# Kernel tuning notes

Hardware: AMD Instinct MI355X
Metric: run time of the kernel (lower is better)

Reference implementation:

```python
import jax, jax.numpy as jnp
import numpy as np

H = 8          # num_heads
KD = 64        # key_dim
R = 256        # num_random_features
EPS = 1e-3     # kernel_epsilon
SCALE = 1.0 / np.sqrt(KD)
CHUNK = 128    # chunk size for causal scan (math identical to full cumsum)


def setup_inputs() -> dict:
    key = jax.random.key(0)
    ks = jax.random.split(key, 7)
    B, S, D = 4, 4096, H * KD
    x = jax.random.normal(ks[0], (B, S, D), dtype=jnp.float32)
    Wq = jax.random.normal(ks[1], (D, D), dtype=jnp.float32) * 0.02
    Wk = jax.random.normal(ks[2], (D, D), dtype=jnp.float32) * 0.02
    Wv = jax.random.normal(ks[3], (D, D), dtype=jnp.float32) * 0.02
    Wo = jax.random.normal(ks[4], (D, D), dtype=jnp.float32) * 0.02
    bo = jnp.zeros((D,), dtype=jnp.float32)
    # random_features: orthogonal rows within each KD block (keras 'orthogonal' init approx)
    g = jax.random.normal(ks[5], (R, KD), dtype=jnp.float32)
    rf = jnp.concatenate([jnp.linalg.qr(b.T)[0].T for b in g.reshape(R // KD, KD, KD)], axis=0)
    return {"x": x, "Wq": Wq, "Wk": Wk, "Wv": Wv, "Wo": Wo, "bo": bo, "rf": rf}


def _kernel_features(z, rf):
    # z: [B,S,H,KD] -> [B,S,H,R]; scale applied AFTER projection as in source
    p = jnp.einsum('bshd,rd->bshr', z, rf) * SCALE
    p = p - jnp.max(p, axis=-1, keepdims=True)
    return jnp.exp(p) + EPS


def _causal_favor(qf, kf, v):
    # qf,kf: [B,S,H,R]; v: [B,S,H,KD]. Equivalent to cumsum of bshrd outer products.
    B, S, _, _ = qf.shape
    nc = S // CHUNK
    def to_chunks(t):
        return jnp.moveaxis(t.reshape(B, nc, CHUNK, *t.shape[2:]), 1, 0)
    qc_all, kc_all, vc_all = to_chunks(qf), to_chunks(kf), to_chunks(v)

    @jax.checkpoint
    def step(carry, inp):
        S0, Z0 = carry                     # S0: [B,H,R,KD], Z0: [B,H,R]
        qc, kc, vc = inp                   # [B,C,H,R], [B,C,H,R], [B,C,H,KD]
        kv = jnp.einsum('bchr,bchd->bchrd', kc, vc)
        kv_cum = jnp.cumsum(kv, axis=1) + S0[:, None]
        num = jnp.einsum('bchr,bchrd->bchd', qc, kv_cum)
        z_cum = jnp.cumsum(kc, axis=1) + Z0[:, None]
        den = jnp.einsum('bchr,bchr->bch', qc, z_cum) + EPS
        out = num / den[..., None]
        return (kv_cum[:, -1], z_cum[:, -1]), out

    S0 = jnp.zeros((B, H, R, KD), dtype=qf.dtype)
    Z0 = jnp.zeros((B, H, R), dtype=qf.dtype)
    _, outs = jax.lax.scan(step, (S0, Z0), (qc_all, kc_all, vc_all))
    return jnp.moveaxis(outs, 0, 1).reshape(B, S, H, KD)


def reference(x, Wq, Wk, Wv, Wo, bo, rf):
    B, S, D = x.shape
    q = (x @ Wq).reshape(B, S, H, KD)
    k = (x @ Wk).reshape(B, S, H, KD)
    v = (x @ Wv).reshape(B, S, H, KD)
    qf = _kernel_features(q, rf)
    kf = _kernel_features(k, rf)
    attn = _causal_favor(qf, kf, v)        # [B,S,H,KD]
    attn = attn.reshape(B, S, H * KD)
    return attn @ Wo + bo
```

## Files before the change

kernel.cpp:

```cpp
#include <hip/hip_runtime.h>
#include <stdint.h>


namespace {
constexpr int kB = 4;
constexpr int kS = 4096;
constexpr int kH = 8;
constexpr int kD = 512;
constexpr int kR = 256;
constexpr int kNC = 32;
constexpr float kEPS = 1e-3f;
constexpr int kSP = 80;
constexpr int kSST = kSP * 256;
}

typedef __attribute__((ext_vector_type(8))) short bf16x8;
typedef __attribute__((ext_vector_type(4))) float f32x4;

__device__ __forceinline__ f32x4 mfma16(bf16x8 a, bf16x8 b, f32x4 c) {
  return __builtin_amdgcn_mfma_f32_16x16x32_bf16(a, b, c, 0, 0, 0);
}

__device__ __forceinline__ uint16_t f2bf(float x) {
  union { float f; uint32_t i; } c; c.f = x;
  uint32_t r = c.i + 0x7fffu + ((c.i >> 16) & 1u);
  return (uint16_t)(r >> 16);
}

__global__ __launch_bounds__(256) void cast_inputs(
    const float* __restrict__ x, const float* __restrict__ rfm,
    uint16_t* __restrict__ x16, uint16_t* __restrict__ rf16)
{
  int i4 = blockIdx.x * 256 + threadIdx.x;
  const int n1 = 2097152;
  const int n2 = 4096;
  const float* src; uint16_t* dst; int off;
  if (i4 < n1) { src = x; dst = x16; off = i4; }
  else if (i4 < n1 + n2) { src = rfm; dst = rf16; off = i4 - n1; }
  else return;
  float4 v = *(const float4*)(src + (size_t)off * 4);
  uint2 o;
  o.x = (uint32_t)f2bf(v.x) | ((uint32_t)f2bf(v.y) << 16);
  o.y = (uint32_t)f2bf(v.z) | ((uint32_t)f2bf(v.w) << 16);
  *(uint2*)(dst + (size_t)off * 4) = o;
}

__global__ __launch_bounds__(256) void transpose_w(
    const float* __restrict__ Wq, const float* __restrict__ Wk,
    const float* __restrict__ Wv, const float* __restrict__ Wo,
    uint16_t* __restrict__ WtBase)
{
  __shared__ uint16_t t16[64][72];
  const int z = blockIdx.z;
  const float* W = (z == 0) ? Wq : (z == 1) ? Wk : (z == 2) ? Wv : Wo;
  uint16_t* Wt = WtBase + (size_t)z * 262144;
  const int tid = threadIdx.x;
  const int k0 = blockIdx.x * 64, n0 = blockIdx.y * 64;
#pragma unroll
  for (int i = 0; i < 4; ++i) {
    int idx = tid + 256 * i;
    int kk = idx >> 4, nn4 = (idx & 15) * 4;
    float4 v = *(const float4*)(W + (size_t)(k0 + kk) * 512 + n0 + nn4);
    t16[kk][nn4 + 0] = f2bf(v.x);
    t16[kk][nn4 + 1] = f2bf(v.y);
    t16[kk][nn4 + 2] = f2bf(v.z);
    t16[kk][nn4 + 3] = f2bf(v.w);
  }
  __syncthreads();
#pragma unroll
  for (int i = 0; i < 4; ++i) {
    int idx = tid + 256 * i;
    int nn = idx >> 4, kk4 = (idx & 15) * 4;
    uint2 o;
    o.x = (uint32_t)t16[kk4 + 0][nn] | ((uint32_t)t16[kk4 + 1][nn] << 16);
    o.y = (uint32_t)t16[kk4 + 2][nn] | ((uint32_t)t16[kk4 + 3][nn] << 16);
    *(uint2*)(Wt + (size_t)(n0 + nn) * 512 + k0 + kk4) = o;
  }
}

template <bool BF16OUT>
__global__ __launch_bounds__(256) void gemm_bf16(
    const uint16_t* __restrict__ A, const uint16_t* __restrict__ Bt,
    const float* __restrict__ bias, void* __restrict__ O)
{
  const int tid = threadIdx.x;
  const int w = tid >> 6, lane = tid & 63;
  const int lr = lane & 15, lg = lane >> 4;
  const int m_base = blockIdx.x * 128 + w * 32;
  const int n_base = blockIdx.y * 64;

  f32x4 acc[2][4];
#pragma unroll
  for (int mf = 0; mf < 2; ++mf)
#pragma unroll
    for (int nf = 0; nf < 4; ++nf) acc[mf][nf] = (f32x4){0.f, 0.f, 0.f, 0.f};

  const uint16_t* a0p = A + (size_t)(m_base + lr) * 512 + 8 * lg;
  const uint16_t* a1p = a0p + (size_t)16 * 512;
  const uint16_t* bp = Bt + (size_t)(n_base + lr) * 512 + 8 * lg;

#pragma unroll
  for (int ks = 0; ks < 16; ++ks) {
    bf16x8 a0 = *(const bf16x8*)(a0p + ks * 32);
    bf16x8 a1 = *(const bf16x8*)(a1p + ks * 32);
#pragma unroll
    for (int nf = 0; nf < 4; ++nf) {
      bf16x8 b = *(const bf16x8*)(bp + (size_t)nf * 16 * 512 + ks * 32);
      acc[0][nf] = mfma16(a0, b, acc[0][nf]);
      acc[1][nf] = mfma16(a1, b, acc[1][nf]);
    }
  }

  float badd[4];
#pragma unroll
  for (int nf = 0; nf < 4; ++nf)
    badd[nf] = bias ? bias[n_base + nf * 16 + lr] : 0.0f;

  if constexpr (BF16OUT) {
    __shared__ uint16_t tr[4][32][72];
#pragma unroll
    for (int mf = 0; mf < 2; ++mf)
#pragma unroll
      for (int nf = 0; nf < 4; ++nf)
#pragma unroll
        for (int reg = 0; reg < 4; ++reg)
          tr[w][mf * 16 + 4 * lg + reg][nf * 16 + lr] = f2bf(acc[mf][nf][reg] + badd[nf]);
    __syncthreads();
#pragma unroll
    for (int it = 0; it < 4; ++it) {
      int idx = it * 64 + lane;
      int row = idx >> 3, c8 = (idx & 7) * 8;
      uint4 val = *(const uint4*)&tr[w][row][c8];
      *(uint4*)((uint16_t*)O + (size_t)(m_base + row) * 512 + n_base + c8) = val;
    }
  } else {
    __shared__ float trf[4][32][68];
#pragma unroll
    for (int mf = 0; mf < 2; ++mf)
#pragma unroll
      for (int nf = 0; nf < 4; ++nf)
#pragma unroll
        for (int reg = 0; reg < 4; ++reg)
          trf[w][mf * 16 + 4 * lg + reg][nf * 16 + lr] = acc[mf][nf][reg] + badd[nf];
    __syncthreads();
#pragma unroll
    for (int it = 0; it < 8; ++it) {
      int idx = it * 64 + lane;
      int row = idx >> 4, c4 = (idx & 15) * 4;
      float4 val = *(const float4*)&trf[w][row][c4];
      *(float4*)((float*)O + (size_t)(m_base + row) * 512 + n_base + c4) = val;
    }
  }
}

__global__ __launch_bounds__(256) void gemm_feat(
    const uint16_t* __restrict__ x16, const uint16_t* __restrict__ WtBase,
    const uint16_t* __restrict__ rf16,
    uint16_t* __restrict__ qf, uint16_t* __restrict__ kf)
{
  __shared__ uint16_t trbuf[4][2176];

  const uint16_t* Bt = WtBase + (size_t)blockIdx.z * 262144;
  uint16_t* dst = blockIdx.z ? kf : qf;
  const int h = blockIdx.y;
  const int tid = threadIdx.x;
  const int w = tid >> 6, lane = tid & 63;
  const int lr = lane & 15, lg = lane >> 4;
  const int m_base = blockIdx.x * 128 + w * 32;

  f32x4 acc[2][4];
#pragma unroll
  for (int mf = 0; mf < 2; ++mf)
#pragma unroll
    for (int nf = 0; nf < 4; ++nf) acc[mf][nf] = (f32x4){0.f, 0.f, 0.f, 0.f};

  const uint16_t* a0p = x16 + (size_t)(m_base + lr) * 512 + 8 * lg;
  const uint16_t* a1p = a0p + (size_t)16 * 512;
  const uint16_t* bp = Bt + (size_t)(h * 64 + lr) * 512 + 8 * lg;

#pragma unroll
  for (int ks = 0; ks < 16; ++ks) {
    bf16x8 a0 = *(const bf16x8*)(a0p + ks * 32);
    bf16x8 a1 = *(const bf16x8*)(a1p + ks * 32);
#pragma unroll
    for (int nf = 0; nf < 4; ++nf) {
      bf16x8 b = *(const bf16x8*)(bp + (size_t)nf * 16 * 512 + ks * 32);
      acc[0][nf] = mfma16(a0, b, acc[0][nf]);
      acc[1][nf] = mfma16(a1, b, acc[1][nf]);
    }
  }

  uint16_t (*trw)[72] = (uint16_t (*)[72])&trbuf[w][0];
  bf16x8 qa[2][2];
#pragma unroll
  for (int mf = 0; mf < 2; ++mf) {
#pragma unroll
    for (int nf = 0; nf < 4; ++nf)
#pragma unroll
      for (int reg = 0; reg < 4; ++reg)
        trw[4 * lg + reg][nf * 16 + lr] = f2bf(acc[mf][nf][reg] * 0.125f);
    qa[mf][0] = *(const bf16x8*)&trw[lr][8 * lg];
    qa[mf][1] = *(const bf16x8*)&trw[lr][32 + 8 * lg];
  }

  f32x4 acc2[2][16];
#pragma unroll
  for (int mf = 0; mf < 2; ++mf)
#pragma unroll
    for (int nf = 0; nf < 16; ++nf) acc2[mf][nf] = (f32x4){0.f, 0.f, 0.f, 0.f};
#pragma unroll
  for (int ks = 0; ks < 2; ++ks) {
#pragma unroll
    for (int nf = 0; nf < 16; ++nf) {
      bf16x8 b = *(const bf16x8*)(rf16 + (size_t)(nf * 16 + lr) * 64 + ks * 32 + 8 * lg);
      acc2[0][nf] = mfma16(qa[0][ks], b, acc2[0][nf]);
      acc2[1][nf] = mfma16(qa[1][ks], b, acc2[1][nf]);
    }
  }

  uint16_t (*trh)[136] = (uint16_t (*)[136])&trbuf[w][0];
#pragma unroll
  for (int mf = 0; mf < 2; ++mf) {
    float mx[4] = {-1e30f, -1e30f, -1e30f, -1e30f};
#pragma unroll
    for (int nf = 0; nf < 16; ++nf)
#pragma unroll
      for (int reg = 0; reg < 4; ++reg)
        mx[reg] = fmaxf(mx[reg], acc2[mf][nf][reg]);
#pragma unroll
    for (int reg = 0; reg < 4; ++reg) {
      mx[reg] = fmaxf(mx[reg], __shfl_xor(mx[reg], 1));
      mx[reg] = fmaxf(mx[reg], __shfl_xor(mx[reg], 2));
      mx[reg] = fmaxf(mx[reg], __shfl_xor(mx[reg], 4));
      mx[reg] = fmaxf(mx[reg], __shfl_xor(mx[reg], 8));
    }
#pragma unroll
    for (int half = 0; half < 2; ++half) {
#pragma unroll
      for (int nf8 = 0; nf8 < 8; ++nf8) {
        int nf = half * 8 + nf8;
#pragma unroll
        for (int reg = 0; reg < 4; ++reg)
          trh[4 * lg + reg][nf8 * 16 + lr] =
              f2bf(__expf(acc2[mf][nf][reg] - mx[reg]) + kEPS);
      }
#pragma unroll
      for (int it = 0; it < 4; ++it) {
        int idx = it * 64 + lane;
        int row = idx >> 4, c8 = (idx & 15) * 8;
        uint4 val = *(const uint4*)&trh[row][c8];
        size_t t = (size_t)m_base + mf * 16 + row;
        *(uint4*)(dst + (t * 8 + h) * 256 + half * 128 + c8) = val;
      }
    }
  }
}

__global__ __launch_bounds__(256) void chunk_mfma(
    const uint16_t* __restrict__ kfeat, const uint16_t* __restrict__ vbuf,
    uint16_t* __restrict__ Skv)
{
  __shared__ uint16_t Vaug[80][136];
  __shared__ uint16_t uni2[21120];
  uint16_t (*kfT)[72] = (uint16_t (*)[72])uni2;
  uint16_t (*outT)[264] = (uint16_t (*)[264])uni2;

  const int c = blockIdx.x, bh = blockIdx.y;
  const int b = bh >> 3, h = bh & 7;
  const int tid = threadIdx.x;
  const int w = tid >> 6, lane = tid & 63;
  const int lr = lane & 15, lg = lane >> 4;
  const size_t srow = (size_t)b * kS + (size_t)c * 128;

#pragma unroll
  for (int i = 0; i < 4; ++i) {
    int idx = tid + 256 * i;
    int u = idx & 127, d = (idx >> 7) * 8;
    uint4 w8 = *(const uint4*)(vbuf + (srow + u) * kD + h * 64 + d);
    Vaug[d + 0][u] = (uint16_t)(w8.x & 0xffff);
    Vaug[d + 1][u] = (uint16_t)(w8.x >> 16);
    Vaug[d + 2][u] = (uint16_t)(w8.y & 0xffff);
    Vaug[d + 3][u] = (uint16_t)(w8.y >> 16);
    Vaug[d + 4][u] = (uint16_t)(w8.z & 0xffff);
    Vaug[d + 5][u] = (uint16_t)(w8.z >> 16);
    Vaug[d + 6][u] = (uint16_t)(w8.w & 0xffff);
    Vaug[d + 7][u] = (uint16_t)(w8.w >> 16);
  }
  if (tid < 128) Vaug[64][tid] = 0x3F80;
  if (tid < 136) {
#pragma unroll
    for (int rr = 65; rr < 80; ++rr) Vaug[rr][tid] = 0;
  }

  f32x4 acc[5][4];
#pragma unroll
  for (int mf = 0; mf < 5; ++mf)
#pragma unroll
    for (int nf = 0; nf < 4; ++nf) acc[mf][nf] = (f32x4){0.f, 0.f, 0.f, 0.f};

  const uint16_t* kp0 = kfeat + (srow * kH + h) * kR;
#pragma unroll
  for (int th = 0; th < 2; ++th) {
    if (th) __syncthreads();
    const uint16_t* kp = kp0 + (size_t)th * 64 * (kH * kR);
#pragma unroll
    for (int i = 0; i < 16; ++i) {
      int idx = tid + 256 * i;
      int t = idx >> 6, c4 = idx & 63;
      uint2 wv = *(const uint2*)(kp + (size_t)t * (kH * kR) + c4 * 4);
      int r = c4 * 4;
      kfT[r + 0][t] = (uint16_t)(wv.x & 0xffff);
      kfT[r + 1][t] = (uint16_t)(wv.x >> 16);
      kfT[r + 2][t] = (uint16_t)(wv.y & 0xffff);
      kfT[r + 3][t] = (uint16_t)(wv.y >> 16);
    }
    __syncthreads();
#pragma unroll
    for (int ks = 0; ks < 2; ++ks) {
      bf16x8 af[5];
#pragma unroll
      for (int mf = 0; mf < 5; ++mf)
        af[mf] = *(const bf16x8*)&Vaug[mf * 16 + lr][th * 64 + ks * 32 + 8 * lg];
#pragma unroll
      for (int nf = 0; nf < 4; ++nf) {
        bf16x8 kb = *(const bf16x8*)&kfT[w * 64 + nf * 16 + lr][ks * 32 + 8 * lg];
#pragma unroll
        for (int mf = 0; mf < 5; ++mf)
          acc[mf][nf] = mfma16(af[mf], kb, acc[mf][nf]);
      }
    }
  }

  __syncthreads();
#pragma unroll
  for (int mf = 0; mf < 5; ++mf)
#pragma unroll
    for (int nf = 0; nf < 4; ++nf)
#pragma unroll
      for (int reg = 0; reg < 4; ++reg)
        outT[mf * 16 + 4 * lg + reg][w * 64 + nf * 16 + lr] = f2bf(acc[mf][nf][reg]);
  __syncthreads();

  uint16_t* So = Skv + ((size_t)bh * kNC + c) * kSST;
#pragma unroll
  for (int it = 0; it < 10; ++it) {
    int idx = tid + 256 * it;
    int row = idx >> 5, c8 = (idx & 31) * 8;
    uint4 val = *(const uint4*)&outT[row][c8];
    *(uint4*)(So + (size_t)row * 256 + c8) = val;
  }
}

__global__ __launch_bounds__(256) void prefix_kernel(uint16_t* __restrict__ Skv)
{
  int e = blockIdx.x * 256 + threadIdx.x;
  int bh = e / kSST;
  int rd = e - bh * kSST;
  size_t base = (size_t)bh * kNC * kSST + rd;
  float run = 0.f;
  for (int c = 0; c < kNC; ++c) {
    size_t idx = base + (size_t)c * kSST;
    union { uint32_t i; float f; } cv; cv.i = ((uint32_t)Skv[idx]) << 16;
    Skv[idx] = f2bf(run);
    run += cv.f;
  }
}

__global__ __launch_bounds__(256) void favor_mfma(
    const uint16_t* __restrict__ qfeat, const uint16_t* __restrict__ kfeat,
    const uint16_t* __restrict__ vbuf, const uint16_t* __restrict__ Skv,
    uint16_t* __restrict__ attn16)
{
  __shared__ uint16_t Vaug[80][136];
  __shared__ uint16_t A_l[4][32][40];

  const int c = blockIdx.x, bh = blockIdx.y;
  const int b = bh >> 3, h = bh & 7;
  const int tid = threadIdx.x;
  const int w = tid >> 6, lane = tid & 63;
  const int lr = lane & 15, lg = lane >> 4;
  const size_t srow = (size_t)b * kS + (size_t)c * 128;

#pragma unroll
  for (int i = 0; i < 4; ++i) {
    int idx = tid + 256 * i;
    int u = idx & 127, d = (idx >> 7) * 8;
    uint4 w8 = *(const uint4*)(vbuf + (srow + u) * kD + h * 64 + d);
    Vaug[d + 0][u] = (uint16_t)(w8.x & 0xffff);
    Vaug[d + 1][u] = (uint16_t)(w8.x >> 16);
    Vaug[d + 2][u] = (uint16_t)(w8.y & 0xffff);
    Vaug[d + 3][u] = (uint16_t)(w8.y >> 16);
    Vaug[d + 4][u] = (uint16_t)(w8.z & 0xffff);
    Vaug[d + 5][u] = (uint16_t)(w8.z >> 16);
    Vaug[d + 6][u] = (uint16_t)(w8.w & 0xffff);
    Vaug[d + 7][u] = (uint16_t)(w8.w >> 16);
  }
  if (tid < 128) Vaug[64][tid] = 0x3F80;
  if (tid < 136) {
#pragma unroll
    for (int rr = 65; rr < 80; ++rr) Vaug[rr][tid] = 0;
  }

  bf16x8 qa[2][8];
  const uint16_t* qp = qfeat + ((srow + w * 32 + lr) * kH + h) * kR + 8 * lg;
#pragma unroll
  for (int mf = 0; mf < 2; ++mf)
#pragma unroll
    for (int ks = 0; ks < 8; ++ks)
      qa[mf][ks] = *(const bf16x8*)(qp + (size_t)mf * 16 * (kH * kR) + ks * 32);

  f32x4 o[2][5];
#pragma unroll
  for (int mf = 0; mf < 2; ++mf)
#pragma unroll
    for (int nf = 0; nf < 5; ++nf) o[mf][nf] = (f32x4){0.f, 0.f, 0.f, 0.f};

  const uint16_t* Sg = Skv + ((size_t)bh * kNC + c) * kSST + 8 * lg;
#pragma unroll
  for (int ks = 0; ks < 8; ++ks) {
#pragma unroll
    for (int nf = 0; nf < 5; ++nf) {
      bf16x8 sb = *(const bf16x8*)(Sg + (size_t)(nf * 16 + lr) * 256 + ks * 32);
      o[0][nf] = mfma16(qa[0][ks], sb, o[0][nf]);
      o[1][nf] = mfma16(qa[1][ks], sb, o[1][nf]);
    }
  }

  __syncthreads();

  const uint16_t* kp = kfeat + (srow + lr) * (kH * kR) + h * kR + 8 * lg;
  for (int ut = 0; ut <= w; ++ut) {
    f32x4 aacc[2][2];
#pragma unroll
    for (int mf = 0; mf < 2; ++mf)
#pragma unroll
      for (int nf = 0; nf < 2; ++nf) aacc[mf][nf] = (f32x4){0.f, 0.f, 0.f, 0.f};
#pragma unroll
    for (int ks = 0; ks < 8; ++ks) {
      bf16x8 kb0 = *(const bf16x8*)(kp + (size_t)(ut * 32) * (kH * kR) + ks * 32);
      bf16x8 kb1 = *(const bf16x8*)(kp + (size_t)(ut * 32 + 16) * (kH * kR) + ks * 32);
      aacc[0][0] = mfma16(qa[0][ks], kb0, aacc[0][0]);
      aacc[0][1] = mfma16(qa[0][ks], kb1, aacc[0][1]);
      aacc[1][0] = mfma16(qa[1][ks], kb0, aacc[1][0]);
      aacc[1][1] = mfma16(qa[1][ks], kb1, aacc[1][1]);
    }
#pragma unroll
    for (int mf = 0; mf < 2; ++mf)
#pragma unroll
      for (int nf = 0; nf < 2; ++nf)
#pragma unroll
        for (int reg = 0; reg < 4; ++reg) {
          int trow = mf * 16 + 4 * lg + reg;
          int ucol = nf * 16 + lr;
          float v = aacc[mf][nf][reg];
          if (ut == w && ucol > trow) v = 0.0f;
          A_l[w][trow][ucol] = f2bf(v);
        }
    bf16x8 af0 = *(const bf16x8*)&A_l[w][lr][8 * lg];
    bf16x8 af1 = *(const bf16x8*)&A_l[w][16 + lr][8 * lg];
#pragma unroll
    for (int nf = 0; nf < 5; ++nf) {
      bf16x8 vb = *(const bf16x8*)&Vaug[nf * 16 + lr][ut * 32 + 8 * lg];
      o[0][nf] = mfma16(af0, vb, o[0][nf]);
      o[1][nf] = mfma16(af1, vb, o[1][nf]);
    }
  }

#pragma unroll
  for (int mf = 0; mf < 2; ++mf) {
    float inv[4];
#pragma unroll
    for (int reg = 0; reg < 4; ++reg) {
      float den = __shfl(o[mf][4][reg], lane & 48);
      inv[reg] = 1.0f / (den + kEPS);
    }
    const size_t trow = srow + w * 32 + mf * 16 + 4 * lg;
#pragma unroll
    for (int reg = 0; reg < 4; ++reg) {
      uint16_t* op = attn16 + (trow + reg) * kD + h * 64 + lr;
#pragma unroll
      for (int nf = 0; nf < 4; ++nf)
        op[nf * 16] = f2bf(o[mf][nf][reg] * inv[reg]);
    }
  }
}

extern "C" void kernel_launch(void* const* d_in, const int* in_sizes, int n_in,
                              void* d_out, int out_size, void* d_ws, size_t ws_size,
                              hipStream_t stream)
{
  (void)in_sizes; (void)n_in; (void)out_size; (void)ws_size;
  const float* x  = (const float*)d_in[0];
  const float* Wq = (const float*)d_in[1];
  const float* Wk = (const float*)d_in[2];
  const float* Wv = (const float*)d_in[3];
  const float* Wo = (const float*)d_in[4];
  const float* bo = (const float*)d_in[5];
  const float* rf = (const float*)d_in[6];
  float* out = (float*)d_out;

  const size_t MiB = 1048576;
  char* ws = (char*)d_ws;
  uint16_t* x16    = (uint16_t*)ws;
  uint16_t* attn16 = (uint16_t*)(ws + 16 * MiB);
  uint16_t* v16    = (uint16_t*)(ws + 32 * MiB);
  uint16_t* qf     = (uint16_t*)(ws + 48 * MiB);
  uint16_t* kf     = (uint16_t*)(ws + 112 * MiB);
  uint16_t* Skv    = (uint16_t*)(ws + 176 * MiB);
  uint16_t* Wt     = (uint16_t*)(ws + 216 * MiB);
  uint16_t* rf16   = (uint16_t*)(ws + 218 * MiB);

  cast_inputs<<<dim3(8208, 1, 1), 256, 0, stream>>>(x, rf, x16, rf16);
  transpose_w<<<dim3(8, 8, 4), 256, 0, stream>>>(Wq, Wk, Wv, Wo, Wt);

  gemm_feat<<<dim3(128, 8, 2), 256, 0, stream>>>(x16, Wt, rf16, qf, kf);

  gemm_bf16<true><<<dim3(128, 8, 1), 256, 0, stream>>>(x16, Wt + 2 * 262144, nullptr, v16);

  chunk_mfma<<<dim3(kNC, kB * kH, 1), 256, 0, stream>>>(kf, v16, Skv);
  prefix_kernel<<<dim3(2560, 1, 1), 256, 0, stream>>>(Skv);
  favor_mfma<<<dim3(kNC, kB * kH, 1), 256, 0, stream>>>(qf, kf, v16, Skv, attn16);

  gemm_bf16<false><<<dim3(128, 8, 1), 256, 0, stream>>>(attn16, Wt + 3 * 262144, bo, out);
}
```

Measured before the change: 381.7 us.

## Store q/k features and V head-major; halve feature GEMM tile; stage attn output stores

Moves qf, kf and v16 from a [B,S,H,*] layout to a head-major [B,H,S,*] layout, so the per-(b,h) chunk kernels read contiguous rows instead of rows strided by H. gemm_feat now gives each wave a 16-row tile, so twice as many blocks are launched and fewer accumulator registers are live per thread. favor_mfma now stages its output through shared memory and writes 16-byte coalesced stores instead of scattered 2-byte stores. The x rows in gemm_feat are reused less, and an extra barrier is added before the output stage.

```diff
diff --git a/kernel.cpp b/kernel.cpp
--- a/kernel.cpp
+++ b/kernel.cpp
@@ -126,12 +126,15 @@
         for (int reg = 0; reg < 4; ++reg)
           tr[w][mf * 16 + 4 * lg + reg][nf * 16 + lr] = f2bf(acc[mf][nf][reg] + badd[nf]);
     __syncthreads();
+    const int h = blockIdx.y;
 #pragma unroll
     for (int it = 0; it < 4; ++it) {
       int idx = it * 64 + lane;
       int row = idx >> 3, c8 = (idx & 7) * 8;
       uint4 val = *(const uint4*)&tr[w][row][c8];
-      *(uint4*)((uint16_t*)O + (size_t)(m_base + row) * 512 + n_base + c8) = val;
+      int m = m_base + row;
+      int b = m >> 12, t = m & 4095;
+      *(uint4*)((uint16_t*)O + ((size_t)(b * 8 + h) * 4096 + t) * 64 + c8) = val;
     }
   } else {
     __shared__ float trf[4][32][68];
@@ -158,7 +161,7 @@
     const uint16_t* __restrict__ rf16,
     uint16_t* __restrict__ qf, uint16_t* __restrict__ kf)
 {
-  __shared__ uint16_t trbuf[4][2176];
+  __shared__ uint16_t trbuf[4][16][72];
 
   const uint16_t* Bt = WtBase + (size_t)blockIdx.z * 262144;
   uint16_t* dst = blockIdx.z ? kf : qf;
@@ -166,92 +169,76 @@
   const int tid = threadIdx.x;
   const int w = tid >> 6, lane = tid & 63;
   const int lr = lane & 15, lg = lane >> 4;
-  const int m_base = blockIdx.x * 128 + w * 32;
-
-  f32x4 acc[2][4];
-#pragma unroll
-  for (int mf = 0; mf < 2; ++mf)
-#pragma unroll
-    for (int nf = 0; nf < 4; ++nf) acc[mf][nf] = (f32x4){0.f, 0.f, 0.f, 0.f};
+  const int m_base = blockIdx.x * 64 + w * 16;
+  const int b = m_base >> 12, tloc = m_base & 4095;
+
+  f32x4 acc[4];
+#pragma unroll
+  for (int nf = 0; nf < 4; ++nf) acc[nf] = (f32x4){0.f, 0.f, 0.f, 0.f};
 
   const uint16_t* a0p = x16 + (size_t)(m_base + lr) * 512 + 8 * lg;
-  const uint16_t* a1p = a0p + (size_t)16 * 512;
   const uint16_t* bp = Bt + (size_t)(h * 64 + lr) * 512 + 8 * lg;
 
 #pragma unroll
   for (int ks = 0; ks < 16; ++ks) {
     bf16x8 a0 = *(const bf16x8*)(a0p + ks * 32);
-    bf16x8 a1 = *(const bf16x8*)(a1p + ks * 32);
 #pragma unroll
     for (int nf = 0; nf < 4; ++nf) {
       bf16x8 b = *(const bf16x8*)(bp + (size_t)nf * 16 * 512 + ks * 32);
-      acc[0][nf] = mfma16(a0, b, acc[0][nf]);
-      acc[1][nf] = mfma16(a1, b, acc[1][nf]);
-    }
-  }
-
-  uint16_t (*trw)[72] = (uint16_t (*)[72])&trbuf[w][0];
-  bf16x8 qa[2][2];
-#pragma unroll
-  for (int mf = 0; mf < 2; ++mf) {
-#pragma unroll
-    for (int nf = 0; nf < 4; ++nf)
+      acc[nf] = mfma16(a0, b, acc[nf]);
+    }
+  }
+
+  uint16_t (*trw)[72] = trbuf[w];
+#pragma unroll
+  for (int nf = 0; nf < 4; ++nf)
+#pragma unroll
+    for (int reg = 0; reg < 4; ++reg)
+      trw[4 * lg + reg][nf * 16 + lr] = f2bf(acc[nf][reg] * 0.125f);
+  bf16x8 qa0 = *(const bf16x8*)&trw[lr][8 * lg];
+  bf16x8 qa1 = *(const bf16x8*)&trw[lr][32 + 8 * lg];
+
+  f32x4 acc2[16];
+#pragma unroll
+  for (int nf = 0; nf < 16; ++nf) acc2[nf] = (f32x4){0.f, 0.f, 0.f, 0.f};
+#pragma unroll
+  for (int nf = 0; nf < 16; ++nf) {
+    bf16x8 b0 = *(const bf16x8*)(rf16 + (size_t)(nf * 16 + lr) * 64 + 8 * lg);
+    bf16x8 b1 = *(const bf16x8*)(rf16 + (size_t)(nf * 16 + lr) * 64 + 32 + 8 * lg);
+    acc2[nf] = mfma16(qa0, b0, acc2[nf]);
+    acc2[nf] = mfma16(qa1, b1, acc2[nf]);
+  }
+
+  float mx[4] = {-1e30f, -1e30f, -1e30f, -1e30f};
+#pragma unroll
+  for (int nf = 0; nf < 16; ++nf)
+#pragma unroll
+    for (int reg = 0; reg < 4; ++reg)
+      mx[reg] = fmaxf(mx[reg], acc2[nf][reg]);
+#pragma unroll
+  for (int reg = 0; reg < 4; ++reg) {
+    mx[reg] = fmaxf(mx[reg], __shfl_xor(mx[reg], 1));
+    mx[reg] = fmaxf(mx[reg], __shfl_xor(mx[reg], 2));
+    mx[reg] = fmaxf(mx[reg], __shfl_xor(mx[reg], 4));
+    mx[reg] = fmaxf(mx[reg], __shfl_xor(mx[reg], 8));
+  }
+  uint16_t* dbase = dst + ((size_t)(b * 8 + h) * 4096 + tloc) * 256;
+#pragma unroll
+  for (int qtr = 0; qtr < 4; ++qtr) {
+#pragma unroll
+    for (int nf4 = 0; nf4 < 4; ++nf4) {
+      int nf = qtr * 4 + nf4;
 #pragma unroll
       for (int reg = 0; reg < 4; ++reg)
-        trw[4 * lg + reg][nf * 16 + lr] = f2bf(acc[mf][nf][reg] * 0.125f);
-    qa[mf][0] = *(const bf16x8*)&trw[lr][8 * lg];
-    qa[mf][1] = *(const bf16x8*)&trw[lr][32 + 8 * lg];
-  }
-
-  f32x4 acc2[2][16];
-#pragma unroll
-  for (int mf = 0; mf < 2; ++mf)
-#pragma unroll
-    for (int nf = 0; nf < 16; ++nf) acc2[mf][nf] = (f32x4){0.f, 0.f, 0.f, 0.f};
-#pragma unroll
-  for (int ks = 0; ks < 2; ++ks) {
-#pragma unroll
-    for (int nf = 0; nf < 16; ++nf) {
-      bf16x8 b = *(const bf16x8*)(rf16 + (size_t)(nf * 16 + lr) * 64 + ks * 32 + 8 * lg);
-      acc2[0][nf] = mfma16(qa[0][ks], b, acc2[0][nf]);
-      acc2[1][nf] = mfma16(qa[1][ks], b, acc2[1][nf]);
-    }
-  }
-
-  uint16_t (*trh)[136] = (uint16_t (*)[136])&trbuf[w][0];
-#pragma unroll
-  for (int mf = 0; mf < 2; ++mf) {
-    float mx[4] = {-1e30f, -1e30f, -1e30f, -1e30f};
-#pragma unroll
-    for (int nf = 0; nf < 16; ++nf)
-#pragma unroll
-      for (int reg = 0; reg < 4; ++reg)
-        mx[reg] = fmaxf(mx[reg], acc2[mf][nf][reg]);
-#pragma unroll
-    for (int reg = 0; reg < 4; ++reg) {
-      mx[reg] = fmaxf(mx[reg], __shfl_xor(mx[reg], 1));
-      mx[reg] = fmaxf(mx[reg], __shfl_xor(mx[reg], 2));
-      mx[reg] = fmaxf(mx[reg], __shfl_xor(mx[reg], 4));
-      mx[reg] = fmaxf(mx[reg], __shfl_xor(mx[reg], 8));
-    }
-#pragma unroll
-    for (int half = 0; half < 2; ++half) {
-#pragma unroll
-      for (int nf8 = 0; nf8 < 8; ++nf8) {
-        int nf = half * 8 + nf8;
-#pragma unroll
-        for (int reg = 0; reg < 4; ++reg)
-          trh[4 * lg + reg][nf8 * 16 + lr] =
-              f2bf(__expf(acc2[mf][nf][reg] - mx[reg]) + kEPS);
-      }
-#pragma unroll
-      for (int it = 0; it < 4; ++it) {
-        int idx = it * 64 + lane;
-        int row = idx >> 4, c8 = (idx & 15) * 8;
-        uint4 val = *(const uint4*)&trh[row][c8];
-        size_t t = (size_t)m_base + mf * 16 + row;
-        *(uint4*)(dst + (t * 8 + h) * 256 + half * 128 + c8) = val;
-      }
+        trw[4 * lg + reg][nf4 * 16 + lr] =
+            f2bf(__expf(acc2[nf][reg] - mx[reg]) + kEPS);
+    }
+#pragma unroll
+    for (int it = 0; it < 2; ++it) {
+      int idx = it * 64 + lane;
+      int row = idx >> 3, c8 = (idx & 7) * 8;
+      uint4 val = *(const uint4*)&trw[row][c8];
+      *(uint4*)(dbase + (size_t)row * 256 + qtr * 64 + c8) = val;
     }
   }
 }
@@ -266,17 +253,16 @@
   uint16_t (*outT)[264] = (uint16_t (*)[264])uni2;
 
   const int c = blockIdx.x, bh = blockIdx.y;
-  const int b = bh >> 3, h = bh & 7;
   const int tid = threadIdx.x;
   const int w = tid >> 6, lane = tid & 63;
   const int lr = lane & 15, lg = lane >> 4;
-  const size_t srow = (size_t)b * kS + (size_t)c * 128;
+  const size_t vrow = (size_t)bh * 4096 + (size_t)c * 128;
 
 #pragma unroll
   for (int i = 0; i < 4; ++i) {
     int idx = tid + 256 * i;
     int u = idx & 127, d = (idx >> 7) * 8;
-    uint4 w8 = *(const uint4*)(vbuf + (srow + u) * kD + h * 64 + d);
+    uint4 w8 = *(const uint4*)(vbuf + (vrow + u) * 64 + d);
     Vaug[d + 0][u] = (uint16_t)(w8.x & 0xffff);
     Vaug[d + 1][u] = (uint16_t)(w8.x >> 16);
     Vaug[d + 2][u] = (uint16_t)(w8.y & 0xffff);
@@ -298,16 +284,16 @@
 #pragma unroll
     for (int nf = 0; nf < 4; ++nf) acc[mf][nf] = (f32x4){0.f, 0.f, 0.f, 0.f};
 
-  const uint16_t* kp0 = kfeat + (srow * kH + h) * kR;
+  const uint16_t* kp0 = kfeat + vrow * 256;
 #pragma unroll
   for (int th = 0; th < 2; ++th) {
     if (th) __syncthreads();
-    const uint16_t* kp = kp0 + (size_t)th * 64 * (kH * kR);
+    const uint16_t* kp = kp0 + (size_t)th * 64 * 256;
 #pragma unroll
     for (int i = 0; i < 16; ++i) {
       int idx = tid + 256 * i;
       int t = idx >> 6, c4 = idx & 63;
-      uint2 wv = *(const uint2*)(kp + (size_t)t * (kH * kR) + c4 * 4);
+      uint2 wv = *(const uint2*)(kp + (size_t)t * 256 + c4 * 4);
       int r = c4 * 4;
       kfT[r + 0][t] = (uint16_t)(wv.x & 0xffff);
       kfT[r + 1][t] = (uint16_t)(wv.x >> 16);
@@ -379,13 +365,14 @@
   const int tid = threadIdx.x;
   const int w = tid >> 6, lane = tid & 63;
   const int lr = lane & 15, lg = lane >> 4;
+  const size_t vrow = (size_t)bh * 4096 + (size_t)c * 128;
   const size_t srow = (size_t)b * kS + (size_t)c * 128;
 
 #pragma unroll
   for (int i = 0; i < 4; ++i) {
     int idx = tid + 256 * i;
     int u = idx & 127, d = (idx >> 7) * 8;
-    uint4 w8 = *(const uint4*)(vbuf + (srow + u) * kD + h * 64 + d);
+    uint4 w8 = *(const uint4*)(vbuf + (vrow + u) * 64 + d);
     Vaug[d + 0][u] = (uint16_t)(w8.x & 0xffff);
     Vaug[d + 1][u] = (uint16_t)(w8.x >> 16);
     Vaug[d + 2][u] = (uint16_t)(w8.y & 0xffff);
@@ -402,12 +389,12 @@
   }
 
   bf16x8 qa[2][8];
-  const uint16_t* qp = qfeat + ((srow + w * 32 + lr) * kH + h) * kR + 8 * lg;
+  const uint16_t* qp = qfeat + (vrow + w * 32 + lr) * 256 + 8 * lg;
 #pragma unroll
   for (int mf = 0; mf < 2; ++mf)
 #pragma unroll
     for (int ks = 0; ks < 8; ++ks)
-      qa[mf][ks] = *(const bf16x8*)(qp + (size_t)mf * 16 * (kH * kR) + ks * 32);
+      qa[mf][ks] = *(const bf16x8*)(qp + (size_t)mf * 16 * 256 + ks * 32);
 
   f32x4 o[2][5];
 #pragma unroll
@@ -428,7 +415,7 @@
 
   __syncthreads();
 
-  const uint16_t* kp = kfeat + (srow + lr) * (kH * kR) + h * kR + 8 * lg;
+  const uint16_t* kp = kfeat + (vrow + lr) * 256 + 8 * lg;
   for (int ut = 0; ut <= w; ++ut) {
     f32x4 aacc[2][2];
 #pragma unroll
@@ -437,8 +424,8 @@
       for (int nf = 0; nf < 2; ++nf) aacc[mf][nf] = (f32x4){0.f, 0.f, 0.f, 0.f};
 #pragma unroll
     for (int ks = 0; ks < 8; ++ks) {
-      bf16x8 kb0 = *(const bf16x8*)(kp + (size_t)(ut * 32) * (kH * kR) + ks * 32);
-      bf16x8 kb1 = *(const bf16x8*)(kp + (size_t)(ut * 32 + 16) * (kH * kR) + ks * 32);
+      bf16x8 kb0 = *(const bf16x8*)(kp + (size_t)(ut * 32) * 256 + ks * 32);
+      bf16x8 kb1 = *(const bf16x8*)(kp + (size_t)(ut * 32 + 16) * 256 + ks * 32);
       aacc[0][0] = mfma16(qa[0][ks], kb0, aacc[0][0]);
       aacc[0][1] = mfma16(qa[0][ks], kb1, aacc[0][1]);
       aacc[1][0] = mfma16(qa[1][ks], kb0, aacc[1][0]);
@@ -466,6 +453,8 @@
     }
   }
 
+  __syncthreads();
+  uint16_t (*osc)[72] = (uint16_t (*)[72])&Vaug[0][0];
 #pragma unroll
   for (int mf = 0; mf < 2; ++mf) {
     float inv[4];
@@ -474,14 +463,20 @@
       float den = __shfl(o[mf][4][reg], lane & 48);
       inv[reg] = 1.0f / (den + kEPS);
     }
-    const size_t trow = srow + w * 32 + mf * 16 + 4 * lg;
-#pragma unroll
-    for (int reg = 0; reg < 4; ++reg) {
-      uint16_t* op = attn16 + (trow + reg) * kD + h * 64 + lr;
-#pragma unroll
-      for (int nf = 0; nf < 4; ++nf)
-        op[nf * 16] = f2bf(o[mf][nf][reg] * inv[reg]);
-    }
+#pragma unroll
+    for (int nf = 0; nf < 4; ++nf)
+#pragma unroll
+      for (int reg = 0; reg < 4; ++reg)
+        osc[w * 32 + mf * 16 + 4 * lg + reg][nf * 16 + lr] =
+            f2bf(o[mf][nf][reg] * inv[reg]);
+  }
+  __syncthreads();
+#pragma unroll
+  for (int it = 0; it < 4; ++it) {
+    int idx = tid + 256 * it;
+    int row = idx >> 3, c8 = (idx & 7) * 8;
+    uint4 val = *(const uint4*)&osc[row][c8];
+    *(uint4*)(attn16 + (srow + row) * kD + h * 64 + c8) = val;
   }
 }
 
@@ -513,7 +508,7 @@
   cast_inputs<<<dim3(8208, 1, 1), 256, 0, stream>>>(x, rf, x16, rf16);
   transpose_w<<<dim3(8, 8, 4), 256, 0, stream>>>(Wq, Wk, Wv, Wo, Wt);
 
-  gemm_feat<<<dim3(128, 8, 2), 256, 0, stream>>>(x16, Wt, rf16, qf, kf);
+  gemm_feat<<<dim3(256, 8, 2), 256, 0, stream>>>(x16, Wt, rf16, qf, kf);
 
   gemm_bf16<true><<<dim3(128, 8, 1), 256, 0, stream>>>(x16, Wt + 2 * 262144, nullptr, v16);
 
```

Measured after the change: 432.2 us. 13.2% more time.
